# Performance work log

Hardware: AMD Instinct MI355X
Metric: run time of the kernel (lower is better)

## Reference

```python
import jax, jax.numpy as jnp
import numpy as np

K = 16  # kNN size (self included)
R = 4   # upsampling ratio


def _knn(pts, k):
    # pts: (B,N,3) -> idx (B,N,k); smallest distance first, so idx[:,:,0] is self
    sq = jnp.sum(pts * pts, axis=-1)
    d = sq[:, :, None] - 2.0 * jnp.einsum('bnd,bmd->bnm', pts, pts) + sq[:, None, :]
    _, idx = jax.lax.top_k(-d, k)
    return idx


def _gather(feats, idx):
    # feats (B,N,C), idx (B,N,k) -> (B,N,k,C)
    return jax.vmap(lambda f, i: f[i])(feats, idx)


def _conv1d(x, w, b):  # pointwise Conv1d: x (B,C,N)
    return jnp.einsum('oc,bcn->bon', w, x) + b[None, :, None]


def _conv2d(x, w, b):  # pointwise Conv2d: x (B,C,N,K)
    return jnp.einsum('oc,bcnk->bonk', w, x) + b[None, :, None, None]


def setup_inputs() -> dict:
    key = jax.random.key(0)
    ks = jax.random.split(key, 16)
    B, N = 2, 8192
    w = lambda k, s: jax.random.normal(k, s, jnp.float32) * 0.1
    return {
        'x': jax.random.normal(ks[0], (B, 3, N), jnp.float32),
        'mlp1_w1': w(ks[1], (32, 3)), 'mlp1_b1': jnp.zeros((32,), jnp.float32),
        'mlp1_w2': w(ks[2], (64, 32)), 'mlp1_b2': jnp.zeros((64,), jnp.float32),
        'mlp2_w1': w(ks[3], (32, 9)), 'mlp2_b1': jnp.zeros((32,), jnp.float32),
        'mlp3_w1': w(ks[4], (128, 96)), 'mlp3_b1': jnp.zeros((128,), jnp.float32),
        'mlp3_w2': w(ks[5], (12, 128)), 'mlp3_b2': jnp.zeros((12,), jnp.float32),
        'att_w1': w(ks[6], (128, 64)), 'att_b1': jnp.zeros((128,), jnp.float32),
        'att_w2': w(ks[7], (64, 128)), 'att_b2': jnp.zeros((64,), jnp.float32),
    }


def reference(x, mlp1_w1, mlp1_b1, mlp1_w2, mlp1_b2, mlp2_w1, mlp2_b1,
              mlp3_w1, mlp3_b1, mlp3_w2, mlp3_b2,
              att_w1, att_b1, att_w2, att_b2):
    B, C, N = x.shape
    pts = jnp.transpose(x, (0, 2, 1))                     # (B,N,3)
    idx = _knn(jax.lax.stop_gradient(pts), K)             # (B,N,K)

    # local 3x3 covariance features -> (B,9,N)
    nb = _gather(pts, idx)                                # (B,N,K,3)
    c = nb - jnp.mean(nb, axis=2, keepdims=True)
    cov = jnp.einsum('bnki,bnkj->bnij', c, c) / K         # (B,N,3,3)
    cov_feat = jnp.transpose(cov.reshape(B, N, 9), (0, 2, 1))

    # mlp1: 3 -> 32 -> 64, relu on both (last_act=True)
    f1 = jax.nn.relu(_conv1d(jax.nn.relu(_conv1d(x, mlp1_w1, mlp1_b1)), mlp1_w2, mlp1_b2))

    # gather neighbor features (exclude self) and form relative features
    fk = _gather(jnp.transpose(f1, (0, 2, 1)), idx[:, :, 1:])   # (B,N,K-1,64)
    f_knn = jnp.transpose(fk, (0, 3, 1, 2)) - f1[:, :, :, None]  # (B,64,N,K-1)

    # attention MLP (2D): 64 -> 128 -> 64, softmax over neighbor axis
    h = jax.nn.relu(_conv2d(f_knn, att_w1, att_b1))
    w = jax.nn.softmax(_conv2d(h, att_w2, att_b2), axis=-1)
    f_agg = jnp.sum(w * f_knn, axis=-1)                   # (B,64,N)

    # mlp2: 9 -> 32 with relu
    f_cov = jax.nn.relu(_conv1d(cov_feat, mlp2_w1, mlp2_b1))     # (B,32,N)

    f = jnp.concatenate([f_agg, f_cov], axis=1)           # (B,96,N)
    g = _conv1d(jax.nn.relu(_conv1d(f, mlp3_w1, mlp3_b1)), mlp3_w2, mlp3_b2)  # (B,3R,N)

    return jnp.tile(x, (1, 1, R)) + 0.15 * g.reshape(B, -1, R * N)
```

## Files before the change

### kernel.cpp

```cpp
#include <hip/hip_runtime.h>

#define BB 2
#define NN 8192
#define KK 16
#define QPB 64
#define PRE2 128
#define SLICE 512
#define STASH 32
#define EPSF 0.02f
typedef unsigned long long ull;
typedef unsigned short ushort;
#define KINF 0xFFFFFFFFFFFFFFFFULL
#define BFONE 0x3F80

typedef __attribute__((ext_vector_type(8))) short short8;
typedef __attribute__((ext_vector_type(4))) float f32x4;

static __device__ __forceinline__ ushort f2bf(float f) {
    unsigned u = __float_as_uint(f);
    unsigned r = (u + 0x7FFFu + ((u >> 16) & 1u)) >> 16;
    return (ushort)r;
}
static __device__ __forceinline__ float bf2f(ushort s) {
    return __uint_as_float(((unsigned)s) << 16);
}

static __device__ __forceinline__ float distq(const float4& qp, const float4& cn) {
    return fmaf(qp.x, cn.x, fmaf(qp.y, cn.y, fmaf(qp.z, cn.z, __fadd_rn(qp.w, cn.w))));
}

__global__ __launch_bounds__(256) void prep_f1_kernel(
    const float* __restrict__ x, float4* __restrict__ pts4, float4* __restrict__ pts4n,
    ushort* __restrict__ ptsC64,
    const float* __restrict__ w1, const float* __restrict__ b1,
    const float* __restrict__ w2, const float* __restrict__ b2,
    ushort* __restrict__ f1)
{
    if (blockIdx.x < 64) {
        int t = blockIdx.x * 256 + threadIdx.x;
        int b = t >> 13, n = t & (NN - 1);
        float x0 = x[(b * 3 + 0) * NN + n];
        float x1 = x[(b * 3 + 1) * NN + n];
        float x2 = x[(b * 3 + 2) * NN + n];
        float sq = fmaf(x2, x2, fmaf(x1, x1, __fmul_rn(x0, x0)));
        pts4[t]  = make_float4(x0, x1, x2, sq);
        pts4n[t] = make_float4(-2.f * x0, -2.f * x1, -2.f * x2, sq);

        float m2x = -2.f * x0, m2y = -2.f * x1, m2z = -2.f * x2;
        ushort hx = f2bf(m2x), hy = f2bf(m2y), hz = f2bf(m2z);
        ushort lx = f2bf(m2x - bf2f(hx));
        ushort ly = f2bf(m2y - bf2f(hy));
        ushort lz = f2bf(m2z - bf2f(hz));
        ushort sh = f2bf(sq), sl = f2bf(sq - bf2f(sh));
        short8 r0 = { (short)hx, (short)hy, (short)hz, (short)lx,
                      (short)ly, (short)lz, (short)hx, (short)hy };
        short8 r1 = { (short)hz, (short)lx, (short)ly, (short)lz,
                      (short)sh, (short)sl, (short)BFONE, (short)BFONE };
        short8 zz = { 0, 0, 0, 0, 0, 0, 0, 0 };
        ushort* cp = ptsC64 + (size_t)t * 32;
        *(short8*)(cp)      = r0;
        *(short8*)(cp + 8)  = r1;
        *(short8*)(cp + 16) = zz;
        *(short8*)(cp + 24) = zz;
    } else {
        int P = (blockIdx.x - 64) * 256 + threadIdx.x;
        int b = P >> 13, n = P & (NN - 1);
        float x0 = x[(b * 3 + 0) * NN + n];
        float x1 = x[(b * 3 + 1) * NN + n];
        float x2 = x[(b * 3 + 2) * NN + n];
        float h[32];
#pragma unroll
        for (int o = 0; o < 32; ++o) {
            float v = fmaf(w1[o * 3 + 2], x2, fmaf(w1[o * 3 + 1], x1, fmaf(w1[o * 3 + 0], x0, b1[o])));
            h[o] = fmaxf(v, 0.f);
        }
#pragma unroll
        for (int o4 = 0; o4 < 16; ++o4) {
            float vv[4];
#pragma unroll
            for (int u = 0; u < 4; ++u) {
                int o = o4 * 4 + u;
                float v = b2[o];
#pragma unroll
                for (int k = 0; k < 32; ++k) v = fmaf(w2[o * 32 + k], h[k], v);
                vv[u] = fmaxf(v, 0.f);
            }
            ushort4 s = { f2bf(vv[0]), f2bf(vv[1]), f2bf(vv[2]), f2bf(vv[3]) };
            *(ushort4*)(f1 + (size_t)P * 64 + o4 * 4) = s;
        }
    }
}

#define DRAIN_TOP4()                                             \
    {                                                            \
        for (int j = 0; j < 11; ++j) {                           \
            if (!__any(j < pend)) break;                         \
            float v = pbuf[j * 1024 + t];                        \
            float k = (j < pend) ? v : 3.0e38f;                  \
            bool b3 = k < l3, b2 = k < l2, b1 = k < l1, b0 = k < l0; \
            l3 = b3 ? (b2 ? l2 : k) : l3;                        \
            l2 = b2 ? (b1 ? l1 : k) : l2;                        \
            l1 = b1 ? (b0 ? l0 : k) : l1;                        \
            l0 = b0 ? k : l0;                                    \
        }                                                        \
    }

__global__ __launch_bounds__(1024, 4) void knn_prefix_kernel(
    const float4* __restrict__ pts4, const float4* __restrict__ pts4n,
    float* __restrict__ thrb)
{
    __shared__ float pbuf[11 * 1024];
    __shared__ float smem[16 * 4 * 64];

    const int t    = threadIdx.x;
    const int wv   = t >> 6;
    const int lane = t & 63;
    const int b    = blockIdx.y;
    const int q    = blockIdx.x * QPB + lane;
    const int sl   = __builtin_amdgcn_readfirstlane(wv);

    const float4 qp = pts4[b * NN + q];
    const float4* __restrict__ cp = pts4n + (size_t)b * NN + (size_t)sl * SLICE;

    float l0 = 3.0e38f, l1 = 3.0e38f, l2 = 3.0e38f, l3 = 3.0e38f;
    float curmax = 3.0e38f;
    int pend = 0;

    float4 ca[8], cb2[8];
#pragma unroll
    for (int u = 0; u < 8; ++u) ca[u] = cp[u];

#pragma unroll 1
    for (int i0 = 0; i0 < PRE2; i0 += 16) {
#pragma unroll
        for (int u = 0; u < 8; ++u) cb2[u] = cp[i0 + 8 + u];
#pragma unroll
        for (int u = 0; u < 8; ++u) {
            float d = distq(qp, ca[u]);
            pbuf[pend * 1024 + t] = d;
            pend += (d < curmax) ? 1 : 0;
        }
        if (__any(pend >= 4)) { DRAIN_TOP4(); pend = 0; curmax = l3; }
        if (i0 + 16 < PRE2) {
#pragma unroll
            for (int u = 0; u < 8; ++u) ca[u] = cp[i0 + 16 + u];
        }
#pragma unroll
        for (int u = 0; u < 8; ++u) {
            float d = distq(qp, cb2[u]);
            pbuf[pend * 1024 + t] = d;
            pend += (d < curmax) ? 1 : 0;
        }
        if (__any(pend >= 4)) { DRAIN_TOP4(); pend = 0; curmax = l3; }
    }
    DRAIN_TOP4();

    __syncthreads();
    smem[(wv * 4 + 0) * 64 + lane] = l0;
    smem[(wv * 4 + 1) * 64 + lane] = l1;
    smem[(wv * 4 + 2) * 64 + lane] = l2;
    smem[(wv * 4 + 3) * 64 + lane] = l3;
    __syncthreads();

    if (t < QPB) {
        float h[16];
        int kc[16];
#pragma unroll
        for (int s = 0; s < 16; ++s) { h[s] = smem[(s * 4) * 64 + t]; kc[s] = 0; }
        float best = 3.0e38f;
        for (int o = 0; o < KK; ++o) {
            best = h[0]; int bs = 0;
#pragma unroll
            for (int s = 1; s < 16; ++s) { if (h[s] < best) { best = h[s]; bs = s; } }
#pragma unroll
            for (int s = 0; s < 16; ++s) {
                if (s == bs) {
                    kc[s]++;
                    h[s] = (kc[s] < 4) ? smem[(s * 4 + kc[s]) * 64 + t] : 3.0e38f;
                }
            }
        }
        thrb[(size_t)b * NN + blockIdx.x * QPB + t] = best;
    }
}

__global__ __launch_bounds__(256) void knn_scan_kernel(
    const float4* __restrict__ pts4, const ushort* __restrict__ ptsC64,
    const float* __restrict__ thrb, unsigned* __restrict__ bufm)
{
    __shared__ __align__(16) char lbuf[10240];

    const int t    = threadIdx.x;
    const int wv   = t >> 6;
    const int lane = t & 63;
    const int l15  = lane & 15, l4 = lane >> 4;
    const int b    = blockIdx.y;
    const int z    = blockIdx.z;
    const int qt   = blockIdx.x * 4 + wv;
    const int qbase = qt * 16;

    const float4 p = pts4[(size_t)b * NN + qbase + l15];
    const ushort qhx = f2bf(p.x), qhy = f2bf(p.y), qhz = f2bf(p.z);
    const ushort qlx = f2bf(p.x - bf2f(qhx));
    const ushort qly = f2bf(p.y - bf2f(qhy));
    const ushort qlz = f2bf(p.z - bf2f(qhz));
    const ushort qsh = f2bf(p.w), qsl = f2bf(p.w - bf2f(qsh));
    short8 qf;
    if (l4 == 0)
        qf = short8{ (short)qhx, (short)qhy, (short)qhz, (short)qhx,
                     (short)qhy, (short)qhz, (short)qlx, (short)qly };
    else if (l4 == 1)
        qf = short8{ (short)qlz, (short)qlx, (short)qly, (short)qlz,
                     (short)BFONE, (short)BFONE, (short)qsh, (short)qsl };
    else
        qf = short8{ 0, 0, 0, 0, 0, 0, 0, 0 };

    const float thrq = thrb[(size_t)b * NN + qbase + l15] * 1.001f + EPSF;

    const uint4* __restrict__ gsrc =
        (const uint4*)(ptsC64 + ((size_t)b * NN + (size_t)z * 1024) * 32);

    unsigned* __restrict__ op =
        bufm + (size_t)(b * NN + qbase + l15) * 256 + z * 32 + l4 * 8;

    uint4 r0 = gsrc[t], r1 = gsrc[t + 256];
    unsigned w4[4];

#pragma unroll 1
    for (int g = 0; g < 8; ++g) {
        __syncthreads();
        *(uint4*)(lbuf + (t >> 2) * 80 + (t & 3) * 16) = r0;
        *(uint4*)(lbuf + ((t + 256) >> 2) * 80 + (t & 3) * 16) = r1;
        if (g < 7) {
            r0 = gsrc[(g + 1) * 512 + t];
            r1 = gsrc[(g + 1) * 512 + t + 256];
        }
        __syncthreads();

        unsigned acc = 0;
#pragma unroll
        for (int i = 0; i < 8; ++i) {
            short8 cf = *(const short8*)(lbuf + (i * 16 + l15) * 80 + l4 * 16);
            f32x4 D = { 0.f, 0.f, 0.f, 0.f };
            D = __builtin_amdgcn_mfma_f32_16x16x32_bf16(cf, qf, D, 0, 0, 0);
            acc = acc * 2u + (unsigned)(D[0] <= thrq);
            acc = acc * 2u + (unsigned)(D[1] <= thrq);
            acc = acc * 2u + (unsigned)(D[2] <= thrq);
            acc = acc * 2u + (unsigned)(D[3] <= thrq);
        }
        w4[g & 3] = acc;
        if ((g & 3) == 3)
            *(uint4*)(op + (g >> 2) * 4) = make_uint4(w4[0], w4[1], w4[2], w4[3]);
    }
}

__global__ __launch_bounds__(256) void knn_select_kernel(
    const float4* __restrict__ pts4, const float4* __restrict__ pts4n,
    const unsigned* __restrict__ bufm,
    int* __restrict__ iout)
{
    __shared__ ull sm3[4][8][8][KK];
    __shared__ ushort stash[STASH][256];

    const int t = threadIdx.x;
    const int wv = t >> 6, lane = t & 63;
    const int qq = lane & 7, hh = lane >> 3;
    const int q  = (blockIdx.x * 4 + wv) * 8 + qq;
    const int b  = q >> 13;

    const float4 qp = pts4[q];
    ull list[KK];
#pragma unroll
    for (int i = 0; i < KK; ++i) list[i] = KINF;

    const unsigned* __restrict__ mrow = bufm + (size_t)q * 256 + hh * 32;
    int pend = 0;
#pragma unroll 1
    for (int g4 = 0; g4 < 8; ++g4) {
        uint4 v = ((const uint4*)mrow)[g4];
        unsigned wsv[4] = { v.x, v.y, v.z, v.w };
#pragma unroll
        for (int j = 0; j < 4; ++j) {
            unsigned w = wsv[j];
            const int W = hh * 32 + g4 * 4 + j;
            const int cb = ((W >> 5) << 10) + ((W & 7) << 7) + (((W >> 3) & 3) << 2);
            while (w) {
                int p = __builtin_ctz(w);
                w &= w - 1;
                int m = 31 - p;
                int id = cb + ((m >> 2) << 4) + (m & 3);
                if (pend < STASH) {
                    stash[pend][t] = (ushort)id;
                    ++pend;
                } else {
                    float d = distq(qp, pts4n[b * NN + id]);
                    unsigned ud = __float_as_uint(d);
                    ud ^= ((unsigned)((int)ud >> 31)) | 0x80000000u;
                    ull k = ((ull)ud << 32) | (unsigned)id;
#pragma unroll
                    for (int i2 = KK - 1; i2 > 0; --i2) {
                        bool c1 = k < list[i2];
                        bool c2 = k < list[i2 - 1];
                        ull nd = c2 ? list[i2 - 1] : k;
                        list[i2] = c1 ? nd : list[i2];
                    }
                    list[0] = (k < list[0]) ? k : list[0];
                }
            }
        }
    }

    for (int j = 0; ; j += 2) {
        if (!__any(j < pend)) break;
        int j1 = j + 1;
        int id0 = stash[(j  < pend) ? j  : 0][t];
        int id1 = stash[(j1 < pend) ? j1 : 0][t];
        float4 cn0 = pts4n[b * NN + id0];
        float4 cn1 = pts4n[b * NN + id1];

        float d0 = distq(qp, cn0);
        unsigned ud0 = __float_as_uint(d0);
        ud0 ^= ((unsigned)((int)ud0 >> 31)) | 0x80000000u;
        ull k0 = (j < pend) ? ((((ull)ud0) << 32) | (unsigned)id0) : KINF;
#pragma unroll
        for (int i2 = KK - 1; i2 > 0; --i2) {
            bool c1 = k0 < list[i2];
            bool c2 = k0 < list[i2 - 1];
            ull nd = c2 ? list[i2 - 1] : k0;
            list[i2] = c1 ? nd : list[i2];
        }
        list[0] = (k0 < list[0]) ? k0 : list[0];

        float d1 = distq(qp, cn1);
        unsigned ud1 = __float_as_uint(d1);
        ud1 ^= ((unsigned)((int)ud1 >> 31)) | 0x80000000u;
        ull k1 = (j1 < pend) ? ((((ull)ud1) << 32) | (unsigned)id1) : KINF;
#pragma unroll
        for (int i2 = KK - 1; i2 > 0; --i2) {
            bool c1 = k1 < list[i2];
            bool c2 = k1 < list[i2 - 1];
            ull nd = c2 ? list[i2 - 1] : k1;
            list[i2] = c1 ? nd : list[i2];
        }
        list[0] = (k1 < list[0]) ? k1 : list[0];
    }

#pragma unroll
    for (int k = 0; k < KK; ++k) sm3[wv][hh][qq][k] = list[k];

    if (hh == 0) {
        ull h[8]; int kc[8];
#pragma unroll
        for (int s = 0; s < 8; ++s) { h[s] = sm3[wv][s][qq][0]; kc[s] = 0; }
        int* op = iout + (size_t)q * KK;
        for (int o = 0; o < KK; ++o) {
            ull best = h[0]; int bs = 0;
#pragma unroll
            for (int s = 1; s < 8; ++s) { if (h[s] < best) { best = h[s]; bs = s; } }
            op[o] = (int)(unsigned)(best & 0xFFFFFFFFULL);
#pragma unroll
            for (int s = 0; s < 8; ++s) {
                if (s == bs) {
                    kc[s]++;
                    h[s] = (kc[s] < KK) ? sm3[wv][s][qq][kc[s]] : KINF;
                }
            }
        }
    }
}

__global__ __launch_bounds__(256, 2) void attn_cov_kernel(
    const ushort* __restrict__ f1, const int* __restrict__ idx,
    const float* __restrict__ aw1, const float* __restrict__ ab1,
    const float* __restrict__ aw2, const float* __restrict__ ab2,
    ushort* __restrict__ fagg,
    const float4* __restrict__ pts4,
    const float* __restrict__ cw, const float* __restrict__ cb,
    ushort* __restrict__ fcov)
{
    __shared__ __align__(16) ushort w1l[128][72];
    __shared__ __align__(16) ushort w2l[64][136];
    __shared__ __align__(16) ushort fkb[4][16][72];
    __shared__ __align__(16) ushort hb[4][16][136];

    const int t = threadIdx.x;

    if (blockIdx.x >= 512) {
        int P = (blockIdx.x - 512) * 256 + t;
        int b = P >> 13;
        const int4* ip4 = (const int4*)(idx + (size_t)P * KK);
        int ids[KK];
#pragma unroll
        for (int g = 0; g < 4; ++g) {
            int4 v = ip4[g];
            ids[g * 4 + 0] = v.x; ids[g * 4 + 1] = v.y;
            ids[g * 4 + 2] = v.z; ids[g * 4 + 3] = v.w;
        }
        float px[KK], py[KK], pz[KK];
#pragma unroll
        for (int k = 0; k < KK; ++k) {
            float4 c = pts4[b * NN + ids[k]];
            px[k] = c.x; py[k] = c.y; pz[k] = c.z;
        }
        float mx = 0.f, my = 0.f, mz = 0.f;
#pragma unroll
        for (int k = 0; k < KK; ++k) { mx += px[k]; my += py[k]; mz += pz[k]; }
        mx *= (1.f / 16.f); my *= (1.f / 16.f); mz *= (1.f / 16.f);
        float c00 = 0, c01 = 0, c02 = 0, c11 = 0, c12 = 0, c22 = 0;
#pragma unroll
        for (int k = 0; k < KK; ++k) {
            float dx = px[k] - mx, dy = py[k] - my, dz = pz[k] - mz;
            c00 = fmaf(dx, dx, c00); c01 = fmaf(dx, dy, c01); c02 = fmaf(dx, dz, c02);
            c11 = fmaf(dy, dy, c11); c12 = fmaf(dy, dz, c12); c22 = fmaf(dz, dz, c22);
        }
        const float inv = 1.f / 16.f;
        float cf[9] = { c00 * inv, c01 * inv, c02 * inv,
                        c01 * inv, c11 * inv, c12 * inv,
                        c02 * inv, c12 * inv, c22 * inv };
        ushort* outp = fcov + (size_t)P * 32;
#pragma unroll
        for (int o = 0; o < 32; ++o) {
            float v = cb[o];
#pragma unroll
            for (int m = 0; m < 9; ++m) v = fmaf(cw[o * 9 + m], cf[m], v);
            outp[o] = f2bf(fmaxf(v, 0.f));
        }
        return;
    }

    const int wv = t >> 6, lane = t & 63;
    const int l15 = lane & 15, qd = lane >> 4;

    for (int i = t; i < 128 * 64; i += 256) {
        int r = i >> 6, c = i & 63;
        w1l[r][c] = f2bf(aw1[i]);
    }
    for (int i = t; i < 64 * 128; i += 256) {
        int r = i >> 7, c = i & 127;
        w2l[r][c] = f2bf(aw2[i]);
    }
    __syncthreads();

    const int W = blockIdx.x * 4 + wv;
    for (int g = 0; g < 8; ++g) {
        const int P = W * 8 + g;
        const int b = P >> 13;

        float fc = bf2f(f1[(size_t)P * 64 + lane]);
        ushort fn[15];
#pragma unroll
        for (int j = 0; j < 15; ++j) {
            int nb = idx[(size_t)P * KK + 1 + j];
            fn[j] = f1[((size_t)b * NN + nb) * 64 + lane];
        }
#pragma unroll
        for (int j = 0; j < 15; ++j) fkb[wv][j][lane] = f2bf(bf2f(fn[j]) - fc);
        fkb[wv][15][lane] = 0;

        short8 a0 = *(const short8*)&fkb[wv][l15][qd * 8];
        short8 a1 = *(const short8*)&fkb[wv][l15][32 + qd * 8];

#pragma unroll
        for (int tile = 0; tile < 8; ++tile) {
            float bv = ab1[tile * 16 + l15];
            f32x4 acc = { bv, bv, bv, bv };
            short8 b0 = *(const short8*)&w1l[tile * 16 + l15][qd * 8];
            short8 b1f = *(const short8*)&w1l[tile * 16 + l15][32 + qd * 8];
            acc = __builtin_amdgcn_mfma_f32_16x16x32_bf16(a0, b0, acc, 0, 0, 0);
            acc = __builtin_amdgcn_mfma_f32_16x16x32_bf16(a1, b1f, acc, 0, 0, 0);
#pragma unroll
            for (int reg = 0; reg < 4; ++reg)
                hb[wv][qd * 4 + reg][tile * 16 + l15] = f2bf(fmaxf(acc[reg], 0.f));
        }

        short8 a2[4];
#pragma unroll
        for (int ks = 0; ks < 4; ++ks)
            a2[ks] = *(const short8*)&hb[wv][l15][ks * 32 + qd * 8];

        f32x4 L[4];
#pragma unroll
        for (int tile = 0; tile < 4; ++tile) {
            float bv = ab2[tile * 16 + l15];
            f32x4 acc = { bv, bv, bv, bv };
#pragma unroll
            for (int ks = 0; ks < 4; ++ks) {
                short8 bf = *(const short8*)&w2l[tile * 16 + l15][ks * 32 + qd * 8];
                acc = __builtin_amdgcn_mfma_f32_16x16x32_bf16(a2[ks], bf, acc, 0, 0, 0);
            }
            L[tile] = acc;
        }

        float fa[4];
#pragma unroll
        for (int tile = 0; tile < 4; ++tile) {
            float m1 = -3.0e38f;
#pragma unroll
            for (int reg = 0; reg < 4; ++reg)
                if (qd * 4 + reg < 15) m1 = fmaxf(m1, L[tile][reg]);
            m1 = fmaxf(m1, __shfl_xor(m1, 16));
            m1 = fmaxf(m1, __shfl_xor(m1, 32));
            float e[4], ssum = 0.f;
#pragma unroll
            for (int reg = 0; reg < 4; ++reg) {
                bool valid = (qd * 4 + reg < 15);
                e[reg] = valid ? __expf(L[tile][reg] - m1) : 0.f;
                ssum += e[reg];
            }
            ssum += __shfl_xor(ssum, 16);
            ssum += __shfl_xor(ssum, 32);
            float part = 0.f;
#pragma unroll
            for (int reg = 0; reg < 4; ++reg) {
                float fkv = bf2f(fkb[wv][qd * 4 + reg][tile * 16 + l15]);
                part = fmaf(e[reg], fkv, part);
            }
            part += __shfl_xor(part, 16);
            part += __shfl_xor(part, 32);
            fa[tile] = part / ssum;
        }
        if (qd == 0) {
#pragma unroll
            for (int tile = 0; tile < 4; ++tile)
                fagg[(size_t)P * 64 + tile * 16 + l15] = f2bf(fa[tile]);
        }
    }
}

__global__ __launch_bounds__(256) void mlp3_kernel(
    const ushort* __restrict__ fagg, const ushort* __restrict__ fcov,
    const float* __restrict__ w1, const float* __restrict__ b1,
    const float* __restrict__ w2, const float* __restrict__ b2,
    const float* __restrict__ x, float* __restrict__ out)
{
    __shared__ __align__(16) ushort fb[4][16][104];
    __shared__ __align__(16) ushort hb[4][16][136];

    const int t = threadIdx.x;
    const int wv = t >> 6, lane = t & 63;
    const int l15 = lane & 15, qd = lane >> 4;

    short8 w1f[8][3];
#pragma unroll
    for (int tile = 0; tile < 8; ++tile)
#pragma unroll
        for (int ks = 0; ks < 3; ++ks) {
            const float* p = w1 + ((size_t)(tile * 16 + l15) * 96 + ks * 32 + qd * 8);
            float4 A = *(const float4*)p, B = *(const float4*)(p + 4);
            short8 f;
            f[0] = f2bf(A.x); f[1] = f2bf(A.y); f[2] = f2bf(A.z); f[3] = f2bf(A.w);
            f[4] = f2bf(B.x); f[5] = f2bf(B.y); f[6] = f2bf(B.z); f[7] = f2bf(B.w);
            w1f[tile][ks] = f;
        }
    short8 w2f[4];
#pragma unroll
    for (int ks = 0; ks < 4; ++ks) {
        short8 f = {};
        if (l15 < 12) {
            const float* p = w2 + ((size_t)l15 * 128 + ks * 32 + qd * 8);
            float4 A = *(const float4*)p, B = *(const float4*)(p + 4);
            f[0] = f2bf(A.x); f[1] = f2bf(A.y); f[2] = f2bf(A.z); f[3] = f2bf(A.w);
            f[4] = f2bf(B.x); f[5] = f2bf(B.y); f[6] = f2bf(B.z); f[7] = f2bf(B.w);
        }
        w2f[ks] = f;
    }

    const int T = blockIdx.x * 4 + wv;

    {
        const int pt = lane >> 2, c4 = lane & 3;
        const ushort* fap = fagg + ((size_t)(T * 16 + pt) * 64 + c4 * 16);
        *(short8*)&fb[wv][pt][c4 * 16]     = *(const short8*)(fap);
        *(short8*)&fb[wv][pt][c4 * 16 + 8] = *(const short8*)(fap + 8);
        const ushort* fcp = fcov + ((size_t)(T * 16 + pt) * 32 + c4 * 8);
        *(short8*)&fb[wv][pt][64 + c4 * 8] = *(const short8*)(fcp);
    }

    short8 a[3];
#pragma unroll
    for (int ks = 0; ks < 3; ++ks)
        a[ks] = *(const short8*)&fb[wv][l15][ks * 32 + qd * 8];

#pragma unroll
    for (int tile = 0; tile < 8; ++tile) {
        float bv = b1[tile * 16 + l15];
        f32x4 acc = { bv, bv, bv, bv };
#pragma unroll
        for (int ks = 0; ks < 3; ++ks)
            acc = __builtin_amdgcn_mfma_f32_16x16x32_bf16(a[ks], w1f[tile][ks], acc, 0, 0, 0);
#pragma unroll
        for (int reg = 0; reg < 4; ++reg)
            hb[wv][qd * 4 + reg][tile * 16 + l15] = f2bf(fmaxf(acc[reg], 0.f));
    }

    short8 a2[4];
#pragma unroll
    for (int ks = 0; ks < 4; ++ks)
        a2[ks] = *(const short8*)&hb[wv][l15][ks * 32 + qd * 8];

    float bv2 = (l15 < 12) ? b2[l15] : 0.f;
    f32x4 acc = { bv2, bv2, bv2, bv2 };
#pragma unroll
    for (int ks = 0; ks < 4; ++ks)
        acc = __builtin_amdgcn_mfma_f32_16x16x32_bf16(a2[ks], w2f[ks], acc, 0, 0, 0);

    if (l15 < 12) {
        const int c = l15 >> 2, rr = l15 & 3;
#pragma unroll
        for (int reg = 0; reg < 4; ++reg) {
            int P = T * 16 + qd * 4 + reg;
            int b = P >> 13, n = P & (NN - 1);
            float xv = x[((size_t)b * 3 + c) * NN + n];
            out[(((size_t)b * 3 + c) * 4 + rr) * NN + n] = xv + 0.15f * acc[reg];
        }
    }
}

extern "C" void kernel_launch(void* const* d_in, const int* in_sizes, int n_in,
                              void* d_out, int out_size, void* d_ws, size_t ws_size,
                              hipStream_t stream)
{
    (void)in_sizes; (void)n_in; (void)out_size; (void)ws_size;
    const float* x    = (const float*)d_in[0];
    const float* m1w1 = (const float*)d_in[1];
    const float* m1b1 = (const float*)d_in[2];
    const float* m1w2 = (const float*)d_in[3];
    const float* m1b2 = (const float*)d_in[4];
    const float* m2w1 = (const float*)d_in[5];
    const float* m2b1 = (const float*)d_in[6];
    const float* m3w1 = (const float*)d_in[7];
    const float* m3b1 = (const float*)d_in[8];
    const float* m3w2 = (const float*)d_in[9];
    const float* m3b2 = (const float*)d_in[10];
    const float* aw1  = (const float*)d_in[11];
    const float* ab1  = (const float*)d_in[12];
    const float* aw2  = (const float*)d_in[13];
    const float* ab2  = (const float*)d_in[14];
    float* out = (float*)d_out;

    char* ws = (char*)d_ws;
    float4* pts4   = (float4*)(ws + 0);
    float4* pts4n  = (float4*)(ws + 262144);
    float*  thrb   = (float*)(ws + 524288);
    int*    idxb   = (int*)  (ws + 589824);
    ushort* ptsC64 = (ushort*)(ws + 1638400);
    unsigned* bufm = (unsigned*)(ws + 2686976);
    ushort* f1b    = (ushort*)(ws + 19464192);
    ushort* fagg   = (ushort*)(ws + 21561344);
    ushort* fcov   = (ushort*)(ws + 23658496);

    prep_f1_kernel<<<128, 256, 0, stream>>>(x, pts4, pts4n, ptsC64, m1w1, m1b1, m1w2, m1b2, f1b);
    knn_prefix_kernel<<<dim3(NN / QPB, BB), 1024, 0, stream>>>(pts4, pts4n, thrb);
    knn_scan_kernel<<<dim3(128, BB, 8), 256, 0, stream>>>(pts4, ptsC64, thrb, bufm);
    knn_select_kernel<<<512, 256, 0, stream>>>(pts4, pts4n, bufm, idxb);
    attn_cov_kernel<<<576, 256, 0, stream>>>(f1b, idxb, aw1, ab1, aw2, ab2, fagg,
                                             pts4, m2w1, m2b1, fcov);
    mlp3_kernel<<<256, 256, 0, stream>>>(fagg, fcov, m3w1, m3b1, m3w2, m3b2, x, out);
}
```

Before: 239.7 us.

## Pre-convert weights to bf16 once and stage kNN prefix candidates in LDS

The prep kernel gains 8 extra blocks that convert the attention and mlp3 weights to bf16 once into workspace. attn_cov and mlp3 then load them with vector short8 reads instead of converting fp32 per block. The kNN prefix kernel now stages its candidate slices into shared memory with a block-wide load and reads from LDS instead of register-prefetching from global memory. The pending buffer shrinks from 11 to 7 slots, which is enough for the new 4-per-flush pattern but adds LDS traffic and a barrier.

```diff
diff --git a/kernel.cpp b/kernel.cpp
--- a/kernel.cpp
+++ b/kernel.cpp
@@ -34,8 +34,27 @@
     ushort* __restrict__ ptsC64,
     const float* __restrict__ w1, const float* __restrict__ b1,
     const float* __restrict__ w2, const float* __restrict__ b2,
-    ushort* __restrict__ f1)
+    ushort* __restrict__ f1,
+    const float* __restrict__ aw1, const float* __restrict__ aw2,
+    const float* __restrict__ m3w1, const float* __restrict__ m3w2,
+    ushort* __restrict__ awb1, ushort* __restrict__ awb2,
+    ushort* __restrict__ m3w1b, ushort* __restrict__ m3w2b)
 {
+    if (blockIdx.x >= 128) {
+        int wt = (blockIdx.x - 128) * 256 + threadIdx.x;
+        for (int c = wt; c < 7552; c += 2048) {
+            int i = c * 4;
+            const float* s; ushort* d; int off;
+            if (i < 8192)       { s = aw1;  d = awb1;  off = i; }
+            else if (i < 16384) { s = aw2;  d = awb2;  off = i - 8192; }
+            else if (i < 28672) { s = m3w1; d = m3w1b; off = i - 16384; }
+            else                { s = m3w2; d = m3w2b; off = i - 28672; }
+            float4 v = *(const float4*)(s + off);
+            ushort4 o = { f2bf(v.x), f2bf(v.y), f2bf(v.z), f2bf(v.w) };
+            *(ushort4*)(d + off) = o;
+        }
+        return;
+    }
     if (blockIdx.x < 64) {
         int t = blockIdx.x * 256 + threadIdx.x;
         int b = t >> 13, n = t & (NN - 1);
@@ -93,7 +112,7 @@
 
 #define DRAIN_TOP4()                                             \
     {                                                            \
-        for (int j = 0; j < 11; ++j) {                           \
+        for (int j = 0; j < 7; ++j) {                            \
             if (!__any(j < pend)) break;                         \
             float v = pbuf[j * 1024 + t];                        \
             float k = (j < pend) ? v : 3.0e38f;                  \
@@ -109,45 +128,44 @@
     const float4* __restrict__ pts4, const float4* __restrict__ pts4n,
     float* __restrict__ thrb)
 {
-    __shared__ float pbuf[11 * 1024];
-    __shared__ float smem[16 * 4 * 64];
+    __shared__ __align__(16) char ldsraw[61440];
+    float4* stage = (float4*)ldsraw;
+    float*  pbuf  = (float*)(ldsraw + 32768);
+    float*  mrg   = (float*)ldsraw;
 
     const int t    = threadIdx.x;
     const int wv   = t >> 6;
     const int lane = t & 63;
     const int b    = blockIdx.y;
     const int q    = blockIdx.x * QPB + lane;
-    const int sl   = __builtin_amdgcn_readfirstlane(wv);
 
     const float4 qp = pts4[b * NN + q];
-    const float4* __restrict__ cp = pts4n + (size_t)b * NN + (size_t)sl * SLICE;
+
+    {
+        int f0 = t, f1 = t + 1024;
+        stage[f0] = pts4n[(size_t)b * NN + ((f0 >> 7) << 9) + (f0 & 127)];
+        stage[f1] = pts4n[(size_t)b * NN + ((f1 >> 7) << 9) + (f1 & 127)];
+    }
+    __syncthreads();
+
+    const float4* __restrict__ cp = stage + wv * 128;
 
     float l0 = 3.0e38f, l1 = 3.0e38f, l2 = 3.0e38f, l3 = 3.0e38f;
     float curmax = 3.0e38f;
     int pend = 0;
 
-    float4 ca[8], cb2[8];
-#pragma unroll
-    for (int u = 0; u < 8; ++u) ca[u] = cp[u];
-
 #pragma unroll 1
-    for (int i0 = 0; i0 < PRE2; i0 += 16) {
-#pragma unroll
-        for (int u = 0; u < 8; ++u) cb2[u] = cp[i0 + 8 + u];
-#pragma unroll
-        for (int u = 0; u < 8; ++u) {
-            float d = distq(qp, ca[u]);
+    for (int i0 = 0; i0 < PRE2; i0 += 8) {
+#pragma unroll
+        for (int u = 0; u < 4; ++u) {
+            float d = distq(qp, cp[i0 + u]);
             pbuf[pend * 1024 + t] = d;
             pend += (d < curmax) ? 1 : 0;
         }
         if (__any(pend >= 4)) { DRAIN_TOP4(); pend = 0; curmax = l3; }
-        if (i0 + 16 < PRE2) {
-#pragma unroll
-            for (int u = 0; u < 8; ++u) ca[u] = cp[i0 + 16 + u];
-        }
-#pragma unroll
-        for (int u = 0; u < 8; ++u) {
-            float d = distq(qp, cb2[u]);
+#pragma unroll
+        for (int u = 4; u < 8; ++u) {
+            float d = distq(qp, cp[i0 + u]);
             pbuf[pend * 1024 + t] = d;
             pend += (d < curmax) ? 1 : 0;
         }
@@ -156,17 +174,17 @@
     DRAIN_TOP4();
 
     __syncthreads();
-    smem[(wv * 4 + 0) * 64 + lane] = l0;
-    smem[(wv * 4 + 1) * 64 + lane] = l1;
-    smem[(wv * 4 + 2) * 64 + lane] = l2;
-    smem[(wv * 4 + 3) * 64 + lane] = l3;
+    mrg[(wv * 4 + 0) * 64 + lane] = l0;
+    mrg[(wv * 4 + 1) * 64 + lane] = l1;
+    mrg[(wv * 4 + 2) * 64 + lane] = l2;
+    mrg[(wv * 4 + 3) * 64 + lane] = l3;
     __syncthreads();
 
     if (t < QPB) {
         float h[16];
         int kc[16];
 #pragma unroll
-        for (int s = 0; s < 16; ++s) { h[s] = smem[(s * 4) * 64 + t]; kc[s] = 0; }
+        for (int s = 0; s < 16; ++s) { h[s] = mrg[(s * 4) * 64 + t]; kc[s] = 0; }
         float best = 3.0e38f;
         for (int o = 0; o < KK; ++o) {
             best = h[0]; int bs = 0;
@@ -176,7 +194,7 @@
             for (int s = 0; s < 16; ++s) {
                 if (s == bs) {
                     kc[s]++;
-                    h[s] = (kc[s] < 4) ? smem[(s * 4 + kc[s]) * 64 + t] : 3.0e38f;
+                    h[s] = (kc[s] < 4) ? mrg[(s * 4 + kc[s]) * 64 + t] : 3.0e38f;
                 }
             }
         }
@@ -371,8 +389,8 @@
 
 __global__ __launch_bounds__(256, 2) void attn_cov_kernel(
     const ushort* __restrict__ f1, const int* __restrict__ idx,
-    const float* __restrict__ aw1, const float* __restrict__ ab1,
-    const float* __restrict__ aw2, const float* __restrict__ ab2,
+    const ushort* __restrict__ awb1, const float* __restrict__ ab1,
+    const ushort* __restrict__ awb2, const float* __restrict__ ab2,
     ushort* __restrict__ fagg,
     const float4* __restrict__ pts4,
     const float* __restrict__ cw, const float* __restrict__ cb,
@@ -431,13 +449,15 @@
     const int wv = t >> 6, lane = t & 63;
     const int l15 = lane & 15, qd = lane >> 4;
 
-    for (int i = t; i < 128 * 64; i += 256) {
+#pragma unroll
+    for (int i = t * 8; i < 128 * 64; i += 256 * 8) {
         int r = i >> 6, c = i & 63;
-        w1l[r][c] = f2bf(aw1[i]);
-    }
-    for (int i = t; i < 64 * 128; i += 256) {
+        *(short8*)&w1l[r][c] = *(const short8*)(awb1 + i);
+    }
+#pragma unroll
+    for (int i = t * 8; i < 64 * 128; i += 256 * 8) {
         int r = i >> 7, c = i & 127;
-        w2l[r][c] = f2bf(aw2[i]);
+        *(short8*)&w2l[r][c] = *(const short8*)(awb2 + i);
     }
     __syncthreads();
 
@@ -529,8 +549,8 @@
 
 __global__ __launch_bounds__(256) void mlp3_kernel(
     const ushort* __restrict__ fagg, const ushort* __restrict__ fcov,
-    const float* __restrict__ w1, const float* __restrict__ b1,
-    const float* __restrict__ w2, const float* __restrict__ b2,
+    const ushort* __restrict__ w1b, const float* __restrict__ b1,
+    const ushort* __restrict__ w2b, const float* __restrict__ b2,
     const float* __restrict__ x, float* __restrict__ out)
 {
     __shared__ __align__(16) ushort fb[4][16][104];
@@ -544,24 +564,14 @@
 #pragma unroll
     for (int tile = 0; tile < 8; ++tile)
 #pragma unroll
-        for (int ks = 0; ks < 3; ++ks) {
-            const float* p = w1 + ((size_t)(tile * 16 + l15) * 96 + ks * 32 + qd * 8);
-            float4 A = *(const float4*)p, B = *(const float4*)(p + 4);
-            short8 f;
-            f[0] = f2bf(A.x); f[1] = f2bf(A.y); f[2] = f2bf(A.z); f[3] = f2bf(A.w);
-            f[4] = f2bf(B.x); f[5] = f2bf(B.y); f[6] = f2bf(B.z); f[7] = f2bf(B.w);
-            w1f[tile][ks] = f;
-        }
+        for (int ks = 0; ks < 3; ++ks)
+            w1f[tile][ks] = *(const short8*)(w1b + ((size_t)(tile * 16 + l15) * 96 + ks * 32 + qd * 8));
     short8 w2f[4];
 #pragma unroll
     for (int ks = 0; ks < 4; ++ks) {
         short8 f = {};
-        if (l15 < 12) {
-            const float* p = w2 + ((size_t)l15 * 128 + ks * 32 + qd * 8);
-            float4 A = *(const float4*)p, B = *(const float4*)(p + 4);
-            f[0] = f2bf(A.x); f[1] = f2bf(A.y); f[2] = f2bf(A.z); f[3] = f2bf(A.w);
-            f[4] = f2bf(B.x); f[5] = f2bf(B.y); f[6] = f2bf(B.z); f[7] = f2bf(B.w);
-        }
+        if (l15 < 12)
+            f = *(const short8*)(w2b + ((size_t)l15 * 128 + ks * 32 + qd * 8));
         w2f[ks] = f;
     }
 
@@ -648,12 +658,17 @@
     ushort* f1b    = (ushort*)(ws + 19464192);
     ushort* fagg   = (ushort*)(ws + 21561344);
     ushort* fcov   = (ushort*)(ws + 23658496);
-
-    prep_f1_kernel<<<128, 256, 0, stream>>>(x, pts4, pts4n, ptsC64, m1w1, m1b1, m1w2, m1b2, f1b);
+    ushort* awb1   = (ushort*)(ws + 24707072);
+    ushort* awb2   = (ushort*)(ws + 24723456);
+    ushort* m3w1b  = (ushort*)(ws + 24739840);
+    ushort* m3w2b  = (ushort*)(ws + 24764416);
+
+    prep_f1_kernel<<<136, 256, 0, stream>>>(x, pts4, pts4n, ptsC64, m1w1, m1b1, m1w2, m1b2, f1b,
+                                            aw1, aw2, m3w1, m3w2, awb1, awb2, m3w1b, m3w2b);
     knn_prefix_kernel<<<dim3(NN / QPB, BB), 1024, 0, stream>>>(pts4, pts4n, thrb);
     knn_scan_kernel<<<dim3(128, BB, 8), 256, 0, stream>>>(pts4, ptsC64, thrb, bufm);
     knn_select_kernel<<<512, 256, 0, stream>>>(pts4, pts4n, bufm, idxb);
-    attn_cov_kernel<<<576, 256, 0, stream>>>(f1b, idxb, aw1, ab1, aw2, ab2, fagg,
+    attn_cov_kernel<<<576, 256, 0, stream>>>(f1b, idxb, awb1, ab1, awb2, ab2, fagg,
                                              pts4, m2w1, m2b1, fcov);
-    mlp3_kernel<<<256, 256, 0, stream>>>(fagg, fcov, m3w1, m3b1, m3w2, m3b2, x, out);
-}
+    mlp3_kernel<<<256, 256, 0, stream>>>(fagg, fcov, m3w1b, m3b1, m3w2b, m3b2, x, out);
+}
```

Result: no change. 235.3 us (-1.8%).
